# Kernel tuning notes

Hardware: AMD Instinct MI355X
Metric: run time of the kernel (lower is better)

## Reference

```python
import jax, jax.numpy as jnp
import numpy as np

B, D, T = 16, 512, 2048
K, C = 8, 1024          # num_codebooks, codebook_size
CH = D // K             # chunk_size = 64
COMMIT = 0.25
EPS = 1e-8


def setup_inputs() -> dict:
    key = jax.random.key(0)
    k1, k2 = jax.random.split(key)
    x = jax.random.normal(k1, (B, D, T), dtype=jnp.float32)
    # kaiming-uniform-ish init for codebooks [K, C, CH]
    bound = float(np.sqrt(6.0 / CH))
    codebooks = jax.random.uniform(k2, (K, C, CH), dtype=jnp.float32,
                                   minval=-bound, maxval=bound)
    return {"x": x, "codebooks": codebooks}


def reference(x, codebooks):
    b, d, t = x.shape
    xc = x.reshape(b, K, CH, t)                       # [B,K,CH,T]
    x_norm = jnp.sum(xc * xc, axis=2)[:, :, None, :]  # [B,K,1,T]
    c_norm = jnp.sum(codebooks * codebooks, axis=2)[None, :, :, None]  # [1,K,C,1]
    cross = -2.0 * jnp.einsum('bkdt,kcd->bkct', xc, codebooks)         # [B,K,C,T]
    distances = x_norm + c_norm + cross
    indices = jnp.argmin(distances, axis=2)           # [B,K,T] int
    # gather nearest codewords -> [B,K,T,CH] -> [B,K,CH,T]
    q = codebooks[jnp.arange(K)[None, :, None], indices]
    q = jnp.transpose(q, (0, 1, 3, 2))                # [B,K,CH,T]
    # per-codebook usage histogram
    kk = jnp.broadcast_to(jnp.arange(K)[None, :, None], indices.shape)
    counts = jnp.zeros((K, C), dtype=jnp.float32).at[kk.ravel(), indices.ravel()].add(1.0)
    avg_probs = counts / (b * t)
    perplexity = jnp.exp(jnp.sum(-avg_probs * jnp.log(avg_probs + EPS), axis=1))
    # commitment losses
    sg = jax.lax.stop_gradient
    codebook_loss = jnp.mean((sg(xc) - q) ** 2)
    encoder_loss = jnp.mean((xc - sg(q)) ** 2)
    commit_loss = codebook_loss + COMMIT * encoder_loss
    # straight-through estimator
    quantized = xc + sg(q - xc)
    return quantized.reshape(b, d, t), commit_loss, perplexity
```

## Files before the change

### kernel.cpp

```cpp
#include <hip/hip_runtime.h>
#include <hip/hip_bf16.h>
#include <math.h>

#define B_   16
#define D_   512
#define T_   2048
#define K_   8
#define C_   1024
#define CH_  64
#define NEL_ (B_ * D_ * T_)
#define QOFF 16777216

#define WS_HCN   0
#define WS_CNT   32768
#define WS_SSE   65536
#define WS_CBS   66048

typedef __attribute__((ext_vector_type(8))) short   short8;
typedef __attribute__((ext_vector_type(8))) __bf16  bf16x8;
typedef __attribute__((ext_vector_type(4))) float   f32x4;
typedef __attribute__((ext_vector_type(4))) int     i32x4;

__device__ __forceinline__ unsigned short f2bf_rne(float f) {
    unsigned u = __builtin_bit_cast(unsigned, f);
    u = u + 0x7FFFu + ((u >> 16) & 1u);
    return (unsigned short)(u >> 16);
}

__device__ __forceinline__ void gload_lds16(const void* gsrc, void* ldst) {
    __builtin_amdgcn_global_load_lds(
        (const __attribute__((address_space(1))) unsigned int*)gsrc,
        (__attribute__((address_space(3))) unsigned int*)ldst,
        16, 0, 0);
}

__global__ void vq_prep(const float* __restrict__ cb,
                        unsigned char* __restrict__ cbS,
                        float* __restrict__ hcn,
                        int* __restrict__ counts,
                        double* __restrict__ sse) {
    int g   = blockIdx.x * 256 + threadIdx.x;
    if (g < K_ * C_) counts[g] = 0;
    if (g == 0) *sse = 0.0;

    int row = g >> 3;
    int s8  = g & 7;
    const float* src = cb + (size_t)row * CH_;

    short8 val;
#pragma unroll
    for (int j = 0; j < 8; ++j)
        val[j] = (short)f2bf_rne(-src[s8 * 8 + j]);
    *(short8*)(cbS + (size_t)row * 128 + ((s8 ^ (row & 7)) * 16)) = val;

    if (s8 == 0) {
        float s = 0.f;
#pragma unroll 8
        for (int ch = 0; ch < CH_; ++ch) {
            float v = src[ch];
            s = fmaf(v, v, s);
        }
        hcn[row] = 0.5f * s;
    }
}

#define LDSBUF 16384

__global__ __launch_bounds__(256, 2) void vq_main(
    const float* __restrict__ x,
    const float* __restrict__ cb,
    const unsigned char* __restrict__ cbS,
    const float* __restrict__ hcn,
    float* __restrict__ out,
    int* __restrict__ counts,
    double* __restrict__ sse)
{
    __shared__ __align__(16) unsigned char lds[2 * LDSBUF + 4096 + 1024];
    float* hcnS = (float*)(lds + 2 * LDSBUF);
    int*   idxS = (int*)(lds + 2 * LDSBUF + 4096);

    const int tid  = threadIdx.x;
    const int lane = tid & 63;
    const int wave = tid >> 6;
    const int ln   = lane & 15;
    const int q    = lane >> 4;
    const int q4   = q * 4;

    const int bid = blockIdx.x;
    const int tc  = bid & 7;
    const int k   = (bid >> 3) & 7;
    const int b   = bid >> 6;
    const int t0b = tc * 256;
    const int tw  = t0b + wave * 64;

    short8 bh[4][2];
    float  xn[4];
#pragma unroll
    for (int tt = 0; tt < 4; ++tt) {
        int t = tw + tt * 16 + ln;
        float pn = 0.f;
#pragma unroll
        for (int ks = 0; ks < 2; ++ks) {
            const float* xp = x + ((size_t)(b * D_ + k * CH_ + ks * 32 + q * 8)) * T_ + t;
            short8 sh;
#pragma unroll
            for (int j = 0; j < 8; ++j) {
                float v = xp[(size_t)j * T_];
                pn = fmaf(v, v, pn);
                sh[j] = (short)f2bf_rne(v);
            }
            bh[tt][ks] = sh;
        }
        pn += __shfl_xor(pn, 16);
        pn += __shfl_xor(pn, 32);
        xn[tt] = pn;
    }

    const unsigned char* cbS_k = cbS + (size_t)k * C_ * 128;
    const float*         hcn_k = hcn + k * C_;

    for (int i = tid; i < C_; i += 256) hcnS[i] = hcn_k[i];

    {
        const unsigned char* src = cbS_k + wave * 4096 + lane * 16;
        unsigned char* dst = lds + wave * 4096;
#pragma unroll
        for (int i = 0; i < 4; ++i)
            gload_lds16(src + i * 1024, dst + i * 1024);
    }

    float md[4];
    int   mc[4];
#pragma unroll
    for (int tt = 0; tt < 4; ++tt) { md[tt] = INFINITY; mc[tt] = 0; }

    for (int chunk = 0; chunk < 8; ++chunk) {
        __syncthreads();

        if (chunk < 7) {
            const unsigned char* src =
                cbS_k + (size_t)(chunk + 1) * 16384 + wave * 4096 + lane * 16;
            unsigned char* dst = lds + ((chunk + 1) & 1) * LDSBUF + wave * 4096;
#pragma unroll
            for (int i = 0; i < 4; ++i)
                gload_lds16(src + i * 1024, dst + i * 1024);
        }

        const unsigned char* buf = lds + (chunk & 1) * LDSBUF;
#pragma unroll
        for (int sub = 0; sub < 8; ++sub) {
            const unsigned char* rowb = buf + (sub * 16 + ln) * 128;
            f32x4 h4 = *(const f32x4*)(hcnS + chunk * 128 + sub * 16 + q4);
            f32x4 a[4];
#pragma unroll
            for (int tt = 0; tt < 4; ++tt) a[tt] = h4;
#pragma unroll
            for (int ks = 0; ks < 2; ++ks) {
                int cidx = ((ks * 4 + q) ^ (ln & 7)) * 16;
                bf16x8 ah = __builtin_bit_cast(bf16x8, *(const short8*)(rowb + cidx));
#pragma unroll
                for (int tt = 0; tt < 4; ++tt)
                    a[tt] = __builtin_amdgcn_mfma_f32_16x16x32_bf16(
                        ah, __builtin_bit_cast(bf16x8, bh[tt][ks]), a[tt], 0, 0, 0);
            }
            const int j4 = (chunk * 8 + sub) * 4;
#pragma unroll
            for (int tt = 0; tt < 4; ++tt) {
                float m01 = fminf(a[tt][0], a[tt][1]);
                float m23 = fminf(a[tt][2], a[tt][3]);
                float m   = fminf(m01, m23);
                int rw = (m == a[tt][0]) ? 0 :
                         (m == a[tt][1]) ? 1 :
                         (m == a[tt][2]) ? 2 : 3;
                bool lt = m < md[tt];
                md[tt] = lt ? m : md[tt];
                mc[tt] = lt ? (j4 + rw) : mc[tt];
            }
        }
    }

    double waveSse = 0.0;

#pragma unroll
    for (int tt = 0; tt < 4; ++tt) {
        float d1 = md[tt];
        int   c1 = ((mc[tt] >> 2) << 4) + q4 + (mc[tt] & 3);
#pragma unroll
        for (int off = 16; off <= 32; off <<= 1) {
            float ov = __shfl_xor(d1, off);
            int   oc = __shfl_xor(c1, off);
            bool w = (ov < d1) || (ov == d1 && oc < c1);
            d1 = w ? ov : d1;
            c1 = w ? oc : c1;
        }

        if (q == 0) {
            waveSse += (double)(xn[tt] + 2.0f * d1);
            atomicAdd(&counts[k * C_ + c1], 1);
            idxS[wave * 64 + tt * 16 + ln] = c1;
        }
    }

    for (int off = 32; off > 0; off >>= 1) waveSse += __shfl_down(waveSse, off);
    if (lane == 0) atomicAdd(sse, waveSse);

    __syncthreads();

    const float* cb_k = cb + (size_t)k * C_ * CH_;
    i32x4 idx4 = *(const i32x4*)(idxS + 4 * lane);
#pragma unroll
    for (int h = 0; h < 4; ++h) {
        f32x4 g[4];
#pragma unroll
        for (int m = 0; m < 4; ++m)
            g[m] = *(const f32x4*)(cb_k + (size_t)idx4[m] * CH_
                                   + wave * 16 + h * 4);
#pragma unroll
        for (int rr = 0; rr < 4; ++rr) {
            f32x4 v = { g[0][rr], g[1][rr], g[2][rr], g[3][rr] };
            *(f32x4*)(out + ((size_t)(b * D_ + k * CH_ + wave * 16 + h * 4
                                      + rr)) * T_ + t0b + 4 * lane) = v;
        }
    }
}

__global__ void vq_final(const int* __restrict__ counts,
                         const double* __restrict__ sse,
                         float* __restrict__ out) {
    __shared__ double part[4];
    const int tid = threadIdx.x;
    const int k   = blockIdx.x;
    double local = 0.0;
    for (int j = tid; j < C_; j += 256) {
        double p = (double)counts[k * C_ + j] * (1.0 / (double)(B_ * T_));
        local += -p * log(p + 1e-8);
    }
    for (int off = 32; off > 0; off >>= 1) local += __shfl_down(local, off);
    if ((tid & 63) == 0) part[tid >> 6] = local;
    __syncthreads();
    if (tid == 0) {
        double sum = part[0] + part[1] + part[2] + part[3];
        out[QOFF + 1 + k] = (float)exp(sum);
        if (k == 0)
            out[QOFF] = (float)(1.25 * (*sse) / (double)NEL_);
    }
}

extern "C" void kernel_launch(void* const* d_in, const int* in_sizes, int n_in,
                              void* d_out, int out_size, void* d_ws, size_t ws_size,
                              hipStream_t stream) {
    const float* x  = (const float*)d_in[0];
    const float* cb = (const float*)d_in[1];
    float* out = (float*)d_out;

    float*         hcn    = (float*)((char*)d_ws + WS_HCN);
    int*           counts = (int*)((char*)d_ws + WS_CNT);
    double*        sse    = (double*)((char*)d_ws + WS_SSE);
    unsigned char* cbS    = (unsigned char*)((char*)d_ws + WS_CBS);

    vq_prep<<<(K_ * C_ * 8) / 256, 256, 0, stream>>>(cb, cbS, hcn, counts, sse);
    vq_main<<<B_ * K_ * (T_ / 256), 256, 0, stream>>>(x, cb, cbS, hcn,
                                                      out, counts, sse);
    vq_final<<<K_, 256, 0, stream>>>(counts, sse, out);
}
```

Before: 198.2 us.

## Load whole per-codebook image into LDS once with 512-thread blocks

vq_main now uses 512-thread blocks covering 512 timesteps each and loads the full 128 KB bf16 codebook image for codebook k into LDS in one go. This replaces the double-buffered chunk pipeline and its eight barriers. The codebook is read from global memory half as many times overall, and the per-chunk __syncthreads disappear. In exchange only one block fits per CU, the codebook load is no longer overlapped with compute beyond the x loads, and the half-norms are now read from global/L1 each iteration instead of LDS.

Measured after the change: 214.1 us. 8.0% more time.

```diff
diff --git a/kernel.cpp b/kernel.cpp
--- a/kernel.cpp
+++ b/kernel.cpp
@@ -64,9 +64,9 @@
     }
 }
 
-#define LDSBUF 16384
-
-__global__ __launch_bounds__(256, 2) void vq_main(
+#define IMG_BYTES 131072
+
+__global__ __launch_bounds__(512, 1) void vq_main(
     const float* __restrict__ x,
     const float* __restrict__ cb,
     const unsigned char* __restrict__ cbS,
@@ -75,9 +75,8 @@
     int* __restrict__ counts,
     double* __restrict__ sse)
 {
-    __shared__ __align__(16) unsigned char lds[2 * LDSBUF + 4096 + 1024];
-    float* hcnS = (float*)(lds + 2 * LDSBUF);
-    int*   idxS = (int*)(lds + 2 * LDSBUF + 4096);
+    __shared__ __align__(16) unsigned char lds[IMG_BYTES];
+    int* idxS = (int*)lds;
 
     const int tid  = threadIdx.x;
     const int lane = tid & 63;
@@ -87,11 +86,22 @@
     const int q4   = q * 4;
 
     const int bid = blockIdx.x;
-    const int tc  = bid & 7;
-    const int k   = (bid >> 3) & 7;
-    const int b   = bid >> 6;
-    const int t0b = tc * 256;
+    const int tq  = bid & 3;
+    const int k   = (bid >> 2) & 7;
+    const int b   = bid >> 5;
+    const int t0b = tq * 512;
     const int tw  = t0b + wave * 64;
+
+    const unsigned char* cbS_k = cbS + (size_t)k * C_ * 128;
+    const float*         hcn_k = hcn + k * C_;
+
+    {
+        const unsigned char* src = cbS_k + tid * 16;
+        unsigned char*       dst = lds   + tid * 16;
+#pragma unroll
+        for (int i = 0; i < 16; ++i)
+            gload_lds16(src + i * 8192, dst + i * 8192);
+    }
 
     short8 bh[4][2];
     float  xn[4];
@@ -116,71 +126,46 @@
         xn[tt] = pn;
     }
 
-    const unsigned char* cbS_k = cbS + (size_t)k * C_ * 128;
-    const float*         hcn_k = hcn + k * C_;
-
-    for (int i = tid; i < C_; i += 256) hcnS[i] = hcn_k[i];
-
-    {
-        const unsigned char* src = cbS_k + wave * 4096 + lane * 16;
-        unsigned char* dst = lds + wave * 4096;
-#pragma unroll
-        for (int i = 0; i < 4; ++i)
-            gload_lds16(src + i * 1024, dst + i * 1024);
-    }
+    __syncthreads();
 
     float md[4];
     int   mc[4];
 #pragma unroll
     for (int tt = 0; tt < 4; ++tt) { md[tt] = INFINITY; mc[tt] = 0; }
 
-    for (int chunk = 0; chunk < 8; ++chunk) {
-        __syncthreads();
-
-        if (chunk < 7) {
-            const unsigned char* src =
-                cbS_k + (size_t)(chunk + 1) * 16384 + wave * 4096 + lane * 16;
-            unsigned char* dst = lds + ((chunk + 1) & 1) * LDSBUF + wave * 4096;
-#pragma unroll
-            for (int i = 0; i < 4; ++i)
-                gload_lds16(src + i * 1024, dst + i * 1024);
-        }
-
-        const unsigned char* buf = lds + (chunk & 1) * LDSBUF;
-#pragma unroll
-        for (int sub = 0; sub < 8; ++sub) {
-            const unsigned char* rowb = buf + (sub * 16 + ln) * 128;
-            f32x4 h4 = *(const f32x4*)(hcnS + chunk * 128 + sub * 16 + q4);
-            f32x4 a[4];
-#pragma unroll
-            for (int tt = 0; tt < 4; ++tt) a[tt] = h4;
-#pragma unroll
-            for (int ks = 0; ks < 2; ++ks) {
-                int cidx = ((ks * 4 + q) ^ (ln & 7)) * 16;
-                bf16x8 ah = __builtin_bit_cast(bf16x8, *(const short8*)(rowb + cidx));
-#pragma unroll
-                for (int tt = 0; tt < 4; ++tt)
-                    a[tt] = __builtin_amdgcn_mfma_f32_16x16x32_bf16(
-                        ah, __builtin_bit_cast(bf16x8, bh[tt][ks]), a[tt], 0, 0, 0);
-            }
-            const int j4 = (chunk * 8 + sub) * 4;
-#pragma unroll
-            for (int tt = 0; tt < 4; ++tt) {
-                float m01 = fminf(a[tt][0], a[tt][1]);
-                float m23 = fminf(a[tt][2], a[tt][3]);
-                float m   = fminf(m01, m23);
-                int rw = (m == a[tt][0]) ? 0 :
-                         (m == a[tt][1]) ? 1 :
-                         (m == a[tt][2]) ? 2 : 3;
-                bool lt = m < md[tt];
-                md[tt] = lt ? m : md[tt];
-                mc[tt] = lt ? (j4 + rw) : mc[tt];
-            }
+#pragma unroll 4
+    for (int sub = 0; sub < 64; ++sub) {
+        const unsigned char* rowb = lds + (sub * 16 + ln) * 128;
+        f32x4 h4 = *(const f32x4*)(hcn_k + sub * 16 + q4);
+        f32x4 a[4];
+#pragma unroll
+        for (int tt = 0; tt < 4; ++tt) a[tt] = h4;
+#pragma unroll
+        for (int ks = 0; ks < 2; ++ks) {
+            int cidx = ((ks * 4 + q) ^ (ln & 7)) * 16;
+            bf16x8 ah = __builtin_bit_cast(bf16x8, *(const short8*)(rowb + cidx));
+#pragma unroll
+            for (int tt = 0; tt < 4; ++tt)
+                a[tt] = __builtin_amdgcn_mfma_f32_16x16x32_bf16(
+                    ah, __builtin_bit_cast(bf16x8, bh[tt][ks]), a[tt], 0, 0, 0);
+        }
+        const int j4 = sub * 4;
+#pragma unroll
+        for (int tt = 0; tt < 4; ++tt) {
+            float m01 = fminf(a[tt][0], a[tt][1]);
+            float m23 = fminf(a[tt][2], a[tt][3]);
+            float m   = fminf(m01, m23);
+            int rw = (m == a[tt][0]) ? 0 :
+                     (m == a[tt][1]) ? 1 :
+                     (m == a[tt][2]) ? 2 : 3;
+            bool lt = m < md[tt];
+            md[tt] = lt ? m : md[tt];
+            mc[tt] = lt ? (j4 + rw) : mc[tt];
         }
     }
 
     double waveSse = 0.0;
-
+    int c1s[4];
 #pragma unroll
     for (int tt = 0; tt < 4; ++tt) {
         float d1 = md[tt];
@@ -193,11 +178,11 @@
             d1 = w ? ov : d1;
             c1 = w ? oc : c1;
         }
+        c1s[tt] = c1;
 
         if (q == 0) {
             waveSse += (double)(xn[tt] + 2.0f * d1);
             atomicAdd(&counts[k * C_ + c1], 1);
-            idxS[wave * 64 + tt * 16 + ln] = c1;
         }
     }
 
@@ -206,20 +191,31 @@
 
     __syncthreads();
 
+    if (q == 0) {
+#pragma unroll
+        for (int tt = 0; tt < 4; ++tt)
+            idxS[wave * 64 + tt * 16 + ln] = c1s[tt];
+    }
+    __syncthreads();
+
     const float* cb_k = cb + (size_t)k * C_ * CH_;
-    i32x4 idx4 = *(const i32x4*)(idxS + 4 * lane);
-#pragma unroll
-    for (int h = 0; h < 4; ++h) {
-        f32x4 g[4];
-#pragma unroll
-        for (int m = 0; m < 4; ++m)
-            g[m] = *(const f32x4*)(cb_k + (size_t)idx4[m] * CH_
-                                   + wave * 16 + h * 4);
-#pragma unroll
-        for (int rr = 0; rr < 4; ++rr) {
-            f32x4 v = { g[0][rr], g[1][rr], g[2][rr], g[3][rr] };
-            *(f32x4*)(out + ((size_t)(b * D_ + k * CH_ + wave * 16 + h * 4
-                                      + rr)) * T_ + t0b + 4 * lane) = v;
+#pragma unroll
+    for (int seg = 0; seg < 2; ++seg) {
+        const int L = seg * 256 + 4 * lane;
+        i32x4 idx4 = *(const i32x4*)(idxS + L);
+#pragma unroll
+        for (int h = 0; h < 2; ++h) {
+            f32x4 g[4];
+#pragma unroll
+            for (int m = 0; m < 4; ++m)
+                g[m] = *(const f32x4*)(cb_k + (size_t)idx4[m] * CH_
+                                       + wave * 8 + h * 4);
+#pragma unroll
+            for (int rr = 0; rr < 4; ++rr) {
+                f32x4 v = { g[0][rr], g[1][rr], g[2][rr], g[3][rr] };
+                *(f32x4*)(out + ((size_t)(b * D_ + k * CH_ + wave * 8 + h * 4
+                                          + rr)) * T_ + t0b + L) = v;
+            }
         }
     }
 }
@@ -259,7 +255,6 @@
     unsigned char* cbS    = (unsigned char*)((char*)d_ws + WS_CBS);
 
     vq_prep<<<(K_ * C_ * 8) / 256, 256, 0, stream>>>(cb, cbS, hcn, counts, sse);
-    vq_main<<<B_ * K_ * (T_ / 256), 256, 0, stream>>>(x, cb, cbS, hcn,
-                                                      out, counts, sse);
+    vq_main<<<B_ * K_ * 4, 512, 0, stream>>>(x, cb, cbS, hcn, out, counts, sse);
     vq_final<<<K_, 256, 0, stream>>>(counts, sse, out);
 }
```
